# Kernel tuning notes

Hardware: AMD Instinct MI355X
Metric: run time of the kernel (lower is better)

## Reference

```python
import jax, jax.numpy as jnp
import numpy as np

IH, IW = 48, 48           # img_size
C = 256                   # inp == oup
NH, HD = 8, 32            # num_heads, head_dims; inner_dim = 256
HID = 4 * C               # MLP hidden
N = IH * IW               # window size (seq len) = 2304
SCALE = (C // NH) ** -0.5 # (inp_dims // num_heads) ** -0.5
EPS = 1e-5


def _relative_position_index():
    coords = np.stack(np.meshgrid(np.arange(IH), np.arange(IW), indexing='ij'))
    cf = coords.reshape(2, -1)
    rel = (cf[:, :, None] - cf[:, None, :]).transpose(1, 2, 0)
    rel[:, :, 0] += IH - 1
    rel[:, :, 1] += IW - 1
    rel[:, :, 0] *= 2 * IW - 1
    return jnp.asarray(rel.sum(-1).astype(np.int32))  # [N, N]


def setup_inputs() -> dict:
    key = jax.random.key(0)
    ks = jax.random.split(key, 12)
    s = 0.02
    return {
        'x': jax.random.normal(ks[0], (1, IH, IW, C), jnp.float32),
        'gamma1': jnp.ones((C,), jnp.float32),
        'beta1': jnp.zeros((C,), jnp.float32),
        'w_qkv': jax.random.normal(ks[1], (C, 3 * NH * HD), jnp.float32) * s,
        'w_proj': jax.random.normal(ks[2], (NH * HD, C), jnp.float32) * s,
        'b_proj': jnp.zeros((C,), jnp.float32),
        'bias_table': jax.random.normal(ks[3], ((2 * IH - 1) * (2 * IW - 1), NH), jnp.float32) * s,
        'gamma2': jnp.ones((C,), jnp.float32),
        'beta2': jnp.zeros((C,), jnp.float32),
        'w_fc1': jax.random.normal(ks[4], (C, HID), jnp.float32) * s,
        'b_fc1': jnp.zeros((HID,), jnp.float32),
        'w_fc2': jax.random.normal(ks[5], (HID, C), jnp.float32) * s,
        'b_fc2': jnp.zeros((C,), jnp.float32),
        'rel_idx': _relative_position_index(),
    }


def _layernorm(x, g, b):
    mu = jnp.mean(x, axis=-1, keepdims=True)
    var = jnp.mean(jnp.square(x - mu), axis=-1, keepdims=True)
    return (x - mu) * jax.lax.rsqrt(var + EPS) * g + b


def reference(x, gamma1, beta1, w_qkv, w_proj, b_proj, bias_table,
              gamma2, beta2, w_fc1, b_fc1, w_fc2, b_fc2, rel_idx):
    shortcut = x                                   # [1, IH, IW, C]
    t = x.reshape(1, N, C)
    t = _layernorm(t, gamma1, beta1)

    # qkv: [1, N, 3*NH*HD] -> q, k, v each [1, NH, N, HD]
    qkv = (t @ w_qkv).reshape(1, N, 3, NH, HD).transpose(2, 0, 3, 1, 4)
    q, k, v = qkv[0], qkv[1], qkv[2]
    q = q * SCALE

    attn = jnp.einsum('bhnd,bhmd->bhnm', q, k)     # [1, NH, N, N]
    # relative position bias: gather table rows by index -> [NH, N, N]
    bias = bias_table[rel_idx.reshape(-1)].reshape(N, N, NH).transpose(2, 0, 1)
    attn = jax.nn.softmax(attn + bias[None], axis=-1)

    o = jnp.einsum('bhnm,bhmd->bhnd', attn, v)     # [1, NH, N, HD]
    o = o.transpose(0, 2, 1, 3).reshape(1, N, NH * HD)
    o = o @ w_proj + b_proj                        # [1, N, C]

    x = shortcut + o.reshape(1, IH, IW, C)
    shortcut = x

    t = _layernorm(x.reshape(1, N, C), gamma2, beta2)
    t = jax.nn.gelu(t @ w_fc1 + b_fc1, approximate=False) @ w_fc2 + b_fc2
    return shortcut + t.reshape(1, IH, IW, C)
```

## Files before the change

### kernel.cpp

```cpp
#include <hip/hip_runtime.h>
#include <hip/hip_bf16.h>

typedef __bf16 bf16x8 __attribute__((__ext_vector_type__(8)));
typedef __bf16 bf16x4 __attribute__((__ext_vector_type__(4)));
typedef float  f32x4  __attribute__((__ext_vector_type__(4)));

#define MFMA16(a, b, c) __builtin_amdgcn_mfma_f32_16x16x32_bf16((a), (b), (c), 0, 0, 0)

static constexpr int   NSEQ  = 2304;
static constexpr float SCALE = 0.17677669529663687f;
static constexpr float LOG2E = 1.44269504088896340736f;
static constexpr int   KVS   = 6;
static constexpr float DEFER_THR = 11.5f;

#define SWZ(row, colByte) ((row) * 512 + ((colByte) ^ (((row) & 7) << 4)))

__global__ __launch_bounds__(256) void prep_kernel(
    const float* __restrict__ wqkv, const float* __restrict__ wproj,
    const float* __restrict__ wfc1, const float* __restrict__ wfc2,
    const float* __restrict__ btab,
    __hip_bfloat16* __restrict__ oqkv, __hip_bfloat16* __restrict__ oproj,
    __hip_bfloat16* __restrict__ ofc1, __hip_bfloat16* __restrict__ ofc2,
    float* __restrict__ btabT)
{
    int b = blockIdx.x;
    int tid = threadIdx.x;
    if (b >= 768) {
        int base = (b - 768) * 1024;
        for (int k = tid; k < 1024; k += 256) {
            int e = base + k;
            if (e < 72200) { int i = e >> 3, hh = e & 7; btabT[hh * 9025 + i] = btab[e] * LOG2E; }
        }
        return;
    }
    const float* src; __hip_bfloat16* dst; int K, N, t;
    if (b < 192)      { src = wqkv;  dst = oqkv;  K = 256;  N = 768;  t = b;       }
    else if (b < 256) { src = wproj; dst = oproj; K = 256;  N = 256;  t = b - 192; }
    else if (b < 512) { src = wfc1;  dst = ofc1;  K = 256;  N = 1024; t = b - 256; }
    else              { src = wfc2;  dst = ofc2;  K = 1024; N = 256;  t = b - 512; }
    int ntn = N >> 5;
    int tk = t / ntn, tn = t % ntn;
    __shared__ float tile[32][33];
    int tx = tid & 31, ty = tid >> 5;
    #pragma unroll
    for (int r = 0; r < 4; ++r)
        tile[ty + 8 * r][tx] = src[(size_t)(tk * 32 + ty + 8 * r) * N + tn * 32 + tx];
    __syncthreads();
    #pragma unroll
    for (int r = 0; r < 4; ++r)
        dst[(size_t)(tn * 32 + ty + 8 * r) * K + tk * 32 + tx] =
            __float2bfloat16(tile[tx][ty + 8 * r]);
}

__global__ __launch_bounds__(256) void qkv_ln_kernel(
    const float* __restrict__ x, const float* __restrict__ g1,
    const float* __restrict__ b1, const __hip_bfloat16* __restrict__ BT,
    __hip_bfloat16* __restrict__ Qb, __hip_bfloat16* __restrict__ Kb,
    __hip_bfloat16* __restrict__ Vt)
{
    __shared__ char smem[16 * 512];
    int tid = threadIdx.x;
    int bn = blockIdx.x * 64, bm = blockIdx.y * 16;

    {
        int row = tid >> 4, part = tid & 15;
        const float* xr = x + (size_t)(bm + row) * 256 + part * 16;
        float vals[16];
        float s = 0.f, s2 = 0.f;
        #pragma unroll
        for (int i = 0; i < 4; ++i) {
            f32x4 v4 = *reinterpret_cast<const f32x4*>(xr + 4 * i);
            #pragma unroll
            for (int e = 0; e < 4; ++e) {
                vals[4 * i + e] = v4[e];
                s += v4[e]; s2 += v4[e] * v4[e];
            }
        }
        s  += __shfl_xor(s, 1);  s  += __shfl_xor(s, 2);
        s  += __shfl_xor(s, 4);  s  += __shfl_xor(s, 8);
        s2 += __shfl_xor(s2, 1); s2 += __shfl_xor(s2, 2);
        s2 += __shfl_xor(s2, 4); s2 += __shfl_xor(s2, 8);
        float mu   = s * (1.f / 256.f);
        float var  = s2 * (1.f / 256.f) - mu * mu;
        float rstd = rsqrtf(var + 1e-5f);
        #pragma unroll
        for (int i = 0; i < 4; ++i) {
            int c = part * 16 + 4 * i;
            f32x4 gv = *reinterpret_cast<const f32x4*>(g1 + c);
            f32x4 bv = *reinterpret_cast<const f32x4*>(b1 + c);
            bf16x4 pk;
            #pragma unroll
            for (int e = 0; e < 4; ++e)
                pk[e] = (__bf16)((vals[4 * i + e] - mu) * rstd * gv[e] + bv[e]);
            *reinterpret_cast<bf16x4*>(smem + SWZ(row, c * 2)) = pk;
        }
    }
    __syncthreads();

    int w = tid >> 6, lane = tid & 63, l15 = lane & 15, g = lane >> 4;
    f32x4 acc = (f32x4){0.f, 0.f, 0.f, 0.f};
    const __hip_bfloat16* Brow = BT + (size_t)(bn + w * 16 + l15) * 256 + 8 * g;
    bf16x8 p0[2], p1[2];

#define QLOADB(dst, kb) { \
    _Pragma("unroll") for (int ks = 0; ks < 2; ++ks) \
        dst[ks] = *reinterpret_cast<const bf16x8*>(Brow + (kb) + 32 * ks); }
#define QCOMP(src, kb) { \
    _Pragma("unroll") for (int ks = 0; ks < 2; ++ks) { \
        bf16x8 af = *reinterpret_cast<const bf16x8*>(smem + SWZ(l15, 2 * ((kb) + 32 * ks + 8 * g))); \
        acc = MFMA16(af, src[ks], acc); } }

    QLOADB(p0, 0);
    QLOADB(p1, 64);
    QCOMP(p0, 0);
    QLOADB(p0, 128);
    QCOMP(p1, 64);
    QLOADB(p1, 192);
    QCOMP(p0, 128);
    QCOMP(p1, 192);
#undef QLOADB
#undef QCOMP

    if (bn >= 512) {
        __syncthreads();
        float* vtile = (float*)smem;
        #pragma unroll
        for (int j = 0; j < 4; ++j)
            vtile[(4 * g + j) * 65 + w * 16 + l15] = acc[j];
        __syncthreads();
        for (int e = tid; e < 1024; e += 256) {
            int mi = e & 15, ni = e >> 4;
            int n = bn + ni;
            int h = (n >> 5) & 7, d = n & 31;
            Vt[(size_t)(h * 32 + d) * NSEQ + bm + mi] = __float2bfloat16(vtile[mi * 65 + ni]);
        }
        return;
    }
    #pragma unroll
    for (int j = 0; j < 4; ++j) {
        int m = bm + 4 * g + j;
        int n = bn + w * 16 + l15;
        float v = acc[j];
        int which = n >> 8, h = (n >> 5) & 7, d = n & 31;
        if (which == 0) Qb[((size_t)(h * NSEQ + m) << 5) + d] = __float2bfloat16(v * (SCALE * LOG2E));
        else            Kb[((size_t)(h * NSEQ + m) << 5) + d] = __float2bfloat16(v);
    }
}

__global__ __launch_bounds__(256) void attn_kernel(
    const __hip_bfloat16* __restrict__ Q,
    const __hip_bfloat16* __restrict__ Kb,
    const __hip_bfloat16* __restrict__ Vt,
    const float* __restrict__ btabT,
    float* __restrict__ Pm, float* __restrict__ Pl,
    __hip_bfloat16* __restrict__ PO)
{
    __shared__ float bias_l[10 * 96];
    __shared__ __hip_bfloat16 P_lds[4][16][72];

    int bid = blockIdx.x;
    int h = bid / (36 * KVS);
    int r = bid - h * (36 * KVS);
    int qt = r / KVS, kvq = r - qt * KVS;
    int tid = threadIdx.x;
    int w = tid >> 6, lane = tid & 63, l15 = lane & 15, g = lane >> 4;

    int q0 = qt * 64;
    int i1min = q0 / 48, i1max = (q0 + 63) / 48;
    int dimin = i1min - (kvq * 8 + 7);
    int nrow = (i1max - i1min) + 8;

    for (int i = tid; i < nrow * 95; i += 256) {
        int rr = i / 95, cc = i - rr * 95;
        bias_l[rr * 96 + 94 - cc] = btabT[h * 9025 + (dimin + rr + 47) * 95 + cc];
    }
    __syncthreads();

    int qrow = q0 + w * 16 + l15;
    int i1 = qrow / 48, j1 = qrow - i1 * 48;
    int colBase = (i1 - dimin) * 96 + 47 - j1;
    bf16x8 qf = *reinterpret_cast<const bf16x8*>(Q + ((size_t)(h * NSEQ + qrow) << 5) + 8 * g);

    float m_st = -1e30f, l_st = 0.f;
    f32x4 o0 = (f32x4){0.f, 0.f, 0.f, 0.f};
    f32x4 o1 = (f32x4){0.f, 0.f, 0.f, 0.f};
    const f32x4 zero = (f32x4){0.f, 0.f, 0.f, 0.f};
    int kvbase = kvq * 384;

    const __hip_bfloat16* Kbase = Kb + ((size_t)(h * NSEQ + l15) << 5) + 8 * g;

    bf16x8 kf[4], kn[4];
    #pragma unroll
    for (int s = 0; s < 4; ++s)
        kn[s] = *reinterpret_cast<const bf16x8*>(Kbase + ((size_t)(kvbase + 16 * s) << 5));

    for (int t = 0; t < 6; ++t) {
        int kv0 = kvbase + t * 64;
        #pragma unroll
        for (int s = 0; s < 4; ++s) kf[s] = kn[s];
        bf16x8 vf[4];
        #pragma unroll
        for (int u = 0; u < 4; ++u) {
            int dt = u >> 1, hh = u & 1;
            vf[u] = *reinterpret_cast<const bf16x8*>(
                Vt + (size_t)((h << 5) + 16 * dt + l15) * NSEQ + kv0 + 32 * hh + 8 * g);
        }
        if (t < 5) {
            #pragma unroll
            for (int s = 0; s < 4; ++s)
                kn[s] = *reinterpret_cast<const bf16x8*>(
                    Kbase + ((size_t)(kv0 + 64 + 16 * s) << 5));
        }
        f32x4 st[4];
        #pragma unroll
        for (int s = 0; s < 4; ++s)
            st[s] = MFMA16(kf[s], qf, zero);

        float p[4][4];
        float ms[4];
        #pragma unroll
        for (int s = 0; s < 4; ++s) {
            int kvb = kv0 + 16 * s + 4 * g;
            int i2 = kvb / 48;
            int j2b = kvb - 48 * i2;
            int a0 = colBase - 96 * i2 + j2b;
            #pragma unroll
            for (int j = 0; j < 4; ++j) {
                int addr = a0 + j - ((j2b + j >= 48) ? 144 : 0);
                p[s][j] = st[s][j] + bias_l[addr];
            }
            ms[s] = fmaxf(fmaxf(p[s][0], p[s][1]), fmaxf(p[s][2], p[s][3]));
        }
        float mx = fmaxf(fmaxf(ms[0], ms[1]), fmaxf(ms[2], ms[3]));
        float mn = m_st;
        if (!__all(mx <= m_st + DEFER_THR)) {
            float mxf = fmaxf(mx, __shfl_xor(mx, 16));
            mxf = fmaxf(mxf, __shfl_xor(mxf, 32));
            mn = fmaxf(m_st, mxf);
            float sc = exp2f(m_st - mn);
            m_st = mn;
            l_st *= sc;
            float scr[4];
            #pragma unroll
            for (int j = 0; j < 4; ++j) scr[j] = __shfl(sc, 4 * g + j);
            #pragma unroll
            for (int j = 0; j < 4; ++j) { o0[j] *= scr[j]; o1[j] *= scr[j]; }
        }
        float rsum[4];
        #pragma unroll
        for (int s = 0; s < 4; ++s) {
            #pragma unroll
            for (int j = 0; j < 4; ++j) p[s][j] = exp2f(p[s][j] - mn);
            rsum[s] = (p[s][0] + p[s][1]) + (p[s][2] + p[s][3]);
        }
        l_st += (rsum[0] + rsum[1]) + (rsum[2] + rsum[3]);
        #pragma unroll
        for (int s = 0; s < 4; ++s) {
            bf16x4 pk = { (__bf16)p[s][0], (__bf16)p[s][1], (__bf16)p[s][2], (__bf16)p[s][3] };
            *reinterpret_cast<bf16x4*>(&P_lds[w][l15][16 * s + 4 * g]) = pk;
        }
        #pragma unroll
        for (int hh = 0; hh < 2; ++hh) {
            bf16x8 pf = *reinterpret_cast<const bf16x8*>(&P_lds[w][l15][32 * hh + 8 * g]);
            o0 = MFMA16(pf, vf[hh], o0);
            o1 = MFMA16(pf, vf[2 + hh], o1);
        }
    }

    float l_red = l_st + __shfl_xor(l_st, 16);
    l_red += __shfl_xor(l_red, 32);

    size_t mb = (size_t)(kvq * 8 + h) * NSEQ;
    if (g == 0) { Pm[mb + qrow] = m_st; Pl[mb + qrow] = l_red; }
    #pragma unroll
    for (int dt = 0; dt < 2; ++dt)
        #pragma unroll
        for (int j = 0; j < 4; ++j) {
            int row = q0 + w * 16 + 4 * g + j;
            PO[(mb + row) * 32 + 16 * dt + l15] =
                __float2bfloat16(dt == 0 ? o0[j] : o1[j]);
        }
}

__global__ __launch_bounds__(256) void proj_kernel(
    const __hip_bfloat16* __restrict__ PO, const float* __restrict__ Pm,
    const float* __restrict__ Pl, const __hip_bfloat16* __restrict__ BT,
    const float* __restrict__ bproj, const float* __restrict__ x,
    float* __restrict__ x2)
{
    __shared__ char smem[16 * 512];
    int tid = threadIdx.x;
    int q0 = blockIdx.y * 16, bn = blockIdx.x * 64;

    {
        int row = tid >> 4;
        int c0  = (tid & 15) * 16;
        int h = c0 >> 5, d = c0 & 31;
        float m[KVS], l[KVS], a[KVS];
        #pragma unroll
        for (int k = 0; k < KVS; ++k) {
            size_t mb = (size_t)(k * 8 + h) * NSEQ + q0 + row;
            m[k] = Pm[mb]; l[k] = Pl[mb];
        }
        float M = m[0];
        #pragma unroll
        for (int k = 1; k < KVS; ++k) M = fmaxf(M, m[k]);
        float L = 0.f;
        #pragma unroll
        for (int k = 0; k < KVS; ++k) { a[k] = exp2f(m[k] - M); L += a[k] * l[k]; }
        float inv = 1.f / L;
        float o[16];
        #pragma unroll
        for (int e = 0; e < 16; ++e) o[e] = 0.f;
        #pragma unroll
        for (int k = 0; k < KVS; ++k) {
            const __hip_bfloat16* pr = PO + ((size_t)(k * 8 + h) * NSEQ + q0 + row) * 32 + d;
            bf16x8 po0 = *reinterpret_cast<const bf16x8*>(pr);
            bf16x8 po1 = *reinterpret_cast<const bf16x8*>(pr + 8);
            #pragma unroll
            for (int e = 0; e < 8; ++e) {
                o[e]     += a[k] * (float)po0[e];
                o[8 + e] += a[k] * (float)po1[e];
            }
        }
        #pragma unroll
        for (int i = 0; i < 4; ++i) {
            bf16x4 pk;
            #pragma unroll
            for (int e = 0; e < 4; ++e) pk[e] = (__bf16)(o[4 * i + e] * inv);
            *reinterpret_cast<bf16x4*>(smem + SWZ(row, (c0 + 4 * i) * 2)) = pk;
        }
    }
    __syncthreads();

    int w = tid >> 6, lane = tid & 63, l15 = lane & 15, g = lane >> 4;
    f32x4 acc = (f32x4){0.f, 0.f, 0.f, 0.f};
    const __hip_bfloat16* Brow = BT + (size_t)(bn + w * 16 + l15) * 256 + 8 * g;
    bf16x8 p0[2], p1[2];

#define PLOADB(dst, kb) { \
    _Pragma("unroll") for (int ks = 0; ks < 2; ++ks) \
        dst[ks] = *reinterpret_cast<const bf16x8*>(Brow + (kb) + 32 * ks); }
#define PCOMP(src, kb) { \
    _Pragma("unroll") for (int ks = 0; ks < 2; ++ks) { \
        bf16x8 af = *reinterpret_cast<const bf16x8*>(smem + SWZ(l15, 2 * ((kb) + 32 * ks + 8 * g))); \
        acc = MFMA16(af, src[ks], acc); } }

    PLOADB(p0, 0);
    PLOADB(p1, 64);
    PCOMP(p0, 0);
    PLOADB(p0, 128);
    PCOMP(p1, 64);
    PLOADB(p1, 192);
    PCOMP(p0, 128);
    PCOMP(p1, 192);
#undef PLOADB
#undef PCOMP

    #pragma unroll
    for (int j = 0; j < 4; ++j) {
        int m = q0 + 4 * g + j;
        int n = bn + w * 16 + l15;
        x2[(size_t)m * 256 + n] = acc[j] + bproj[n] + x[(size_t)m * 256 + n];
    }
}

__global__ __launch_bounds__(256) void ln_fc1_kernel(
    const float* __restrict__ x2, const float* __restrict__ g2,
    const float* __restrict__ b2, const __hip_bfloat16* __restrict__ BT,
    const float* __restrict__ bfc1, __hip_bfloat16* __restrict__ hb)
{
    __shared__ char smem[32 * 512];
    int tid = threadIdx.x;
    int bn = blockIdx.x * 64, bm = blockIdx.y * 32;

    {
        int row = tid >> 3, part = tid & 7;
        const float* xr = x2 + (size_t)(bm + row) * 256 + part * 32;
        float vals[32];
        float s = 0.f, s2 = 0.f;
        #pragma unroll
        for (int i = 0; i < 8; ++i) {
            f32x4 v4 = *reinterpret_cast<const f32x4*>(xr + 4 * i);
            #pragma unroll
            for (int e = 0; e < 4; ++e) {
                vals[4 * i + e] = v4[e];
                s += v4[e]; s2 += v4[e] * v4[e];
            }
        }
        s  += __shfl_xor(s, 1);  s  += __shfl_xor(s, 2);  s  += __shfl_xor(s, 4);
        s2 += __shfl_xor(s2, 1); s2 += __shfl_xor(s2, 2); s2 += __shfl_xor(s2, 4);
        float mu   = s * (1.f / 256.f);
        float var  = s2 * (1.f / 256.f) - mu * mu;
        float rstd = rsqrtf(var + 1e-5f);
        #pragma unroll
        for (int i = 0; i < 8; ++i) {
            int c = part * 32 + 4 * i;
            f32x4 gv = *reinterpret_cast<const f32x4*>(g2 + c);
            f32x4 bv = *reinterpret_cast<const f32x4*>(b2 + c);
            bf16x4 pk;
            #pragma unroll
            for (int e = 0; e < 4; ++e)
                pk[e] = (__bf16)((vals[4 * i + e] - mu) * rstd * gv[e] + bv[e]);
            *reinterpret_cast<bf16x4*>(smem + SWZ(row, c * 2)) = pk;
        }
    }
    __syncthreads();

    int w = tid >> 6, lane = tid & 63, l15 = lane & 15, g = lane >> 4;
    int wr = w >> 1, wc = w & 1;
    f32x4 acc[2];
    acc[0] = (f32x4){0.f, 0.f, 0.f, 0.f};
    acc[1] = (f32x4){0.f, 0.f, 0.f, 0.f};
    const __hip_bfloat16* Brow = BT + (size_t)(bn + wc * 32 + l15) * 256 + 8 * g;
    bf16x8 p0[2][2], p1[2][2];

#define FLOADB(dst, kb) { \
    _Pragma("unroll") for (int ks = 0; ks < 2; ++ks) \
    _Pragma("unroll") for (int fj = 0; fj < 2; ++fj) \
        dst[ks][fj] = *reinterpret_cast<const bf16x8*>(Brow + (size_t)16 * fj * 256 + (kb) + 32 * ks); }
#define FCOMP(src, kb) { \
    _Pragma("unroll") for (int ks = 0; ks < 2; ++ks) { \
        bf16x8 af = *reinterpret_cast<const bf16x8*>(smem + SWZ(wr * 16 + l15, 2 * ((kb) + 32 * ks + 8 * g))); \
        _Pragma("unroll") for (int fj = 0; fj < 2; ++fj) \
            acc[fj] = MFMA16(af, src[ks][fj], acc[fj]); } }

    FLOADB(p0, 0);
    FLOADB(p1, 64);
    FCOMP(p0, 0);
    FLOADB(p0, 128);
    FCOMP(p1, 64);
    FLOADB(p1, 192);
    FCOMP(p0, 128);
    FCOMP(p1, 192);
#undef FLOADB
#undef FCOMP

    #pragma unroll
    for (int fj = 0; fj < 2; ++fj)
        #pragma unroll
        for (int j = 0; j < 4; ++j) {
            int m = bm + wr * 16 + 4 * g + j;
            int n = bn + wc * 32 + 16 * fj + l15;
            float r = acc[fj][j] + bfc1[n];
            float u = r * (r * r * 0.044715f + 1.f) * -2.302118131f;
            float gl = r / (1.f + exp2f(u));
            hb[(size_t)m * 1024 + n] = __float2bfloat16(gl);
        }
}

template <int KTOT, int FM, int FN, int WR, int WC>
__global__ __launch_bounds__(128) void fc2_kernel(
    const __hip_bfloat16* __restrict__ A,
    const __hip_bfloat16* __restrict__ BT,
    const float* __restrict__ bias,
    const float* __restrict__ resid,
    float* __restrict__ out0)
{
    constexpr int BM = WR * FM * 16, BN = WC * FN * 16;
    constexpr int NCH = KTOT / 64;
    constexpr int NBUF = 4;
    int bm = blockIdx.y * BM, bn = blockIdx.x * BN;
    int tid = threadIdx.x;
    int w = tid >> 6, lane = tid & 63, l15 = lane & 15, g = lane >> 4;
    int wr = w / WC, wc = w % WC;

    f32x4 acc[FM][FN];
    #pragma unroll
    for (int i = 0; i < FM; ++i)
        #pragma unroll
        for (int j = 0; j < FN; ++j) acc[i][j] = (f32x4){0.f, 0.f, 0.f, 0.f};

    const __hip_bfloat16* Arow = A  + (size_t)(bm + wr * FM * 16 + l15) * KTOT + 8 * g;
    const __hip_bfloat16* Brow = BT + (size_t)(bn + wc * FN * 16 + l15) * KTOT + 8 * g;

    bf16x8 ab[NBUF][2][FM], bb[NBUF][2][FN];

#define LOADC(ib, kb) { \
    _Pragma("unroll") for (int ks = 0; ks < 2; ++ks) { \
        _Pragma("unroll") for (int i = 0; i < FM; ++i) \
            ab[ib][ks][i] = *reinterpret_cast<const bf16x8*>(Arow + (size_t)16 * i * KTOT + (kb) + 32 * ks); \
        _Pragma("unroll") for (int j2 = 0; j2 < FN; ++j2) \
            bb[ib][ks][j2] = *reinterpret_cast<const bf16x8*>(Brow + (size_t)16 * j2 * KTOT + (kb) + 32 * ks); } }
#define COMPC(ib) { \
    _Pragma("unroll") for (int ks = 0; ks < 2; ++ks) \
        _Pragma("unroll") for (int i = 0; i < FM; ++i) \
            _Pragma("unroll") for (int j2 = 0; j2 < FN; ++j2) \
                acc[i][j2] = MFMA16(ab[ib][ks][i], bb[ib][ks][j2], acc[i][j2]); }

    #pragma unroll
    for (int ib = 0; ib < NBUF; ++ib) LOADC(ib, 64 * ib);
    #pragma unroll
    for (int t = 0; t < NCH; ++t) {
        COMPC(t % NBUF);
        if (t + NBUF < NCH) LOADC(t % NBUF, 64 * (t + NBUF));
    }
#undef LOADC
#undef COMPC

    #pragma unroll
    for (int fi = 0; fi < FM; ++fi)
    #pragma unroll
    for (int fj = 0; fj < FN; ++fj)
    #pragma unroll
    for (int j = 0; j < 4; ++j) {
        int m = bm + wr * FM * 16 + 16 * fi + 4 * g + j;
        int n = bn + wc * FN * 16 + 16 * fj + l15;
        out0[(size_t)m * 256 + n] = acc[fi][fj][j] + bias[n] + resid[(size_t)m * 256 + n];
    }
}

extern "C" void kernel_launch(void* const* d_in, const int* in_sizes, int n_in,
                              void* d_out, int out_size, void* d_ws, size_t ws_size,
                              hipStream_t stream)
{
    const float* x      = (const float*)d_in[0];
    const float* gamma1 = (const float*)d_in[1];
    const float* beta1  = (const float*)d_in[2];
    const float* w_qkv  = (const float*)d_in[3];
    const float* w_proj = (const float*)d_in[4];
    const float* b_proj = (const float*)d_in[5];
    const float* btab   = (const float*)d_in[6];
    const float* gamma2 = (const float*)d_in[7];
    const float* beta2  = (const float*)d_in[8];
    const float* w_fc1  = (const float*)d_in[9];
    const float* b_fc1  = (const float*)d_in[10];
    const float* w_fc2  = (const float*)d_in[11];
    const float* b_fc2  = (const float*)d_in[12];

    char* ws = (char*)d_ws;
    size_t off = 0;
    auto alloc = [&](size_t bytes) -> void* {
        void* p = ws + off;
        off += (bytes + 255) & ~(size_t)255;
        return p;
    };
    __hip_bfloat16* wqkvT = (__hip_bfloat16*)alloc((size_t)768 * 256 * 2);
    __hip_bfloat16* wprojT= (__hip_bfloat16*)alloc((size_t)256 * 256 * 2);
    __hip_bfloat16* wfc1T = (__hip_bfloat16*)alloc((size_t)1024 * 256 * 2);
    __hip_bfloat16* wfc2T = (__hip_bfloat16*)alloc((size_t)256 * 1024 * 2);
    float*          btabT = (float*)alloc((size_t)8 * 9025 * 4);
    __hip_bfloat16* Qb    = (__hip_bfloat16*)alloc((size_t)8 * NSEQ * 32 * 2);
    __hip_bfloat16* Kbuf  = (__hip_bfloat16*)alloc((size_t)8 * NSEQ * 32 * 2);
    __hip_bfloat16* Vt    = (__hip_bfloat16*)alloc((size_t)8 * 32 * NSEQ * 2);
    float*          x2    = (float*)alloc((size_t)NSEQ * 256 * 4);
    float*          Pm    = (float*)alloc((size_t)KVS * 8 * NSEQ * 4);
    float*          Pl    = (float*)alloc((size_t)KVS * 8 * NSEQ * 4);
    __hip_bfloat16* PO    = (__hip_bfloat16*)alloc((size_t)KVS * 8 * NSEQ * 32 * 2);
    __hip_bfloat16* hb    = (__hip_bfloat16*)alloc((size_t)NSEQ * 1024 * 2);

    prep_kernel<<<dim3(839), dim3(256), 0, stream>>>(
        w_qkv, w_proj, w_fc1, w_fc2, btab, wqkvT, wprojT, wfc1T, wfc2T, btabT);

    qkv_ln_kernel<<<dim3(12, 144), dim3(256), 0, stream>>>(
        x, gamma1, beta1, wqkvT, Qb, Kbuf, Vt);

    attn_kernel<<<dim3(8 * 36 * KVS), dim3(256), 0, stream>>>(
        Qb, Kbuf, Vt, btabT, Pm, Pl, PO);

    proj_kernel<<<dim3(4, 144), dim3(256), 0, stream>>>(
        PO, Pm, Pl, wprojT, b_proj, x, x2);

    ln_fc1_kernel<<<dim3(16, 72), dim3(256), 0, stream>>>(
        x2, gamma2, beta2, wfc1T, b_fc1, hb);

    fc2_kernel<1024, 1, 1, 2, 1><<<dim3(16, 72), dim3(128), 0, stream>>>(
        hb, wfc2T, b_fc2, x2, (float*)d_out);
}
```

Measured before the change: 196.2 us.

## Split attention KV finer, apply bias multiplicatively, split-K fc2 with atomics

Doubles the attention KV split from 6 to 12 chunks, giving more blocks with shorter loops. It also replaces the additive log-domain bias with a precomputed exp(bias) multiplier, so the running max comes from raw scores plus a margin. The fc2 GEMM becomes split-K over four slices that atomically add into an output pre-initialised by ln_fc1 with the residual plus bias. The costs are more partials for the merge step in proj, atomic contention and non-deterministic summation order, and a heuristic margin that could risk overflow for large biases.

After: 218.0 us. 1.11x slower.

```diff
diff --git a/kernel.cpp b/kernel.cpp
--- a/kernel.cpp
+++ b/kernel.cpp
@@ -10,8 +10,9 @@
 static constexpr int   NSEQ  = 2304;
 static constexpr float SCALE = 0.17677669529663687f;
 static constexpr float LOG2E = 1.44269504088896340736f;
-static constexpr int   KVS   = 6;
+static constexpr int   KVS   = 12;
 static constexpr float DEFER_THR = 11.5f;
+static constexpr float BMARGIN   = 0.25f;
 
 #define SWZ(row, colByte) ((row) * 512 + ((colByte) ^ (((row) & 7) << 4)))
 
@@ -29,7 +30,7 @@
         int base = (b - 768) * 1024;
         for (int k = tid; k < 1024; k += 256) {
             int e = base + k;
-            if (e < 72200) { int i = e >> 3, hh = e & 7; btabT[hh * 9025 + i] = btab[e] * LOG2E; }
+            if (e < 72200) { int i = e >> 3, hh = e & 7; btabT[hh * 9025 + i] = expf(btab[e]); }
         }
         return;
     }
@@ -155,7 +156,7 @@
     float* __restrict__ Pm, float* __restrict__ Pl,
     __hip_bfloat16* __restrict__ PO)
 {
-    __shared__ float bias_l[10 * 96];
+    __shared__ float bias_l[6 * 96];
     __shared__ __hip_bfloat16 P_lds[4][16][72];
 
     int bid = blockIdx.x;
@@ -167,8 +168,8 @@
 
     int q0 = qt * 64;
     int i1min = q0 / 48, i1max = (q0 + 63) / 48;
-    int dimin = i1min - (kvq * 8 + 7);
-    int nrow = (i1max - i1min) + 8;
+    int dimin = i1min - (kvq * 4 + 3);
+    int nrow = (i1max - i1min) + 4;
 
     for (int i = tid; i < nrow * 95; i += 256) {
         int rr = i / 95, cc = i - rr * 95;
@@ -185,7 +186,7 @@
     f32x4 o0 = (f32x4){0.f, 0.f, 0.f, 0.f};
     f32x4 o1 = (f32x4){0.f, 0.f, 0.f, 0.f};
     const f32x4 zero = (f32x4){0.f, 0.f, 0.f, 0.f};
-    int kvbase = kvq * 384;
+    int kvbase = kvq * 192;
 
     const __hip_bfloat16* Kbase = Kb + ((size_t)(h * NSEQ + l15) << 5) + 8 * g;
 
@@ -194,7 +195,7 @@
     for (int s = 0; s < 4; ++s)
         kn[s] = *reinterpret_cast<const bf16x8*>(Kbase + ((size_t)(kvbase + 16 * s) << 5));
 
-    for (int t = 0; t < 6; ++t) {
+    for (int t = 0; t < 3; ++t) {
         int kv0 = kvbase + t * 64;
         #pragma unroll
         for (int s = 0; s < 4; ++s) kf[s] = kn[s];
@@ -205,7 +206,7 @@
             vf[u] = *reinterpret_cast<const bf16x8*>(
                 Vt + (size_t)((h << 5) + 16 * dt + l15) * NSEQ + kv0 + 32 * hh + 8 * g);
         }
-        if (t < 5) {
+        if (t < 2) {
             #pragma unroll
             for (int s = 0; s < 4; ++s)
                 kn[s] = *reinterpret_cast<const bf16x8*>(
@@ -216,8 +217,27 @@
         for (int s = 0; s < 4; ++s)
             st[s] = MFMA16(kf[s], qf, zero);
 
-        float p[4][4];
         float ms[4];
+        #pragma unroll
+        for (int s = 0; s < 4; ++s)
+            ms[s] = fmaxf(fmaxf(st[s][0], st[s][1]), fmaxf(st[s][2], st[s][3]));
+        float mx = fmaxf(fmaxf(ms[0], ms[1]), fmaxf(ms[2], ms[3]));
+        float mn = m_st;
+        if (!__all(mx + BMARGIN <= m_st + DEFER_THR)) {
+            float mxf = fmaxf(mx, __shfl_xor(mx, 16));
+            mxf = fmaxf(mxf, __shfl_xor(mxf, 32));
+            mn = fmaxf(m_st, mxf + BMARGIN);
+            float sc = exp2f(m_st - mn);
+            m_st = mn;
+            l_st *= sc;
+            float scr[4];
+            #pragma unroll
+            for (int j = 0; j < 4; ++j) scr[j] = __shfl(sc, 4 * g + j);
+            #pragma unroll
+            for (int j = 0; j < 4; ++j) { o0[j] *= scr[j]; o1[j] *= scr[j]; }
+        }
+        float pp[4][4];
+        float rsum[4];
         #pragma unroll
         for (int s = 0; s < 4; ++s) {
             int kvb = kv0 + 16 * s + 4 * g;
@@ -227,36 +247,14 @@
             #pragma unroll
             for (int j = 0; j < 4; ++j) {
                 int addr = a0 + j - ((j2b + j >= 48) ? 144 : 0);
-                p[s][j] = st[s][j] + bias_l[addr];
+                pp[s][j] = exp2f(st[s][j] - mn) * bias_l[addr];
             }
-            ms[s] = fmaxf(fmaxf(p[s][0], p[s][1]), fmaxf(p[s][2], p[s][3]));
-        }
-        float mx = fmaxf(fmaxf(ms[0], ms[1]), fmaxf(ms[2], ms[3]));
-        float mn = m_st;
-        if (!__all(mx <= m_st + DEFER_THR)) {
-            float mxf = fmaxf(mx, __shfl_xor(mx, 16));
-            mxf = fmaxf(mxf, __shfl_xor(mxf, 32));
-            mn = fmaxf(m_st, mxf);
-            float sc = exp2f(m_st - mn);
-            m_st = mn;
-            l_st *= sc;
-            float scr[4];
-            #pragma unroll
-            for (int j = 0; j < 4; ++j) scr[j] = __shfl(sc, 4 * g + j);
-            #pragma unroll
-            for (int j = 0; j < 4; ++j) { o0[j] *= scr[j]; o1[j] *= scr[j]; }
-        }
-        float rsum[4];
+            rsum[s] = (pp[s][0] + pp[s][1]) + (pp[s][2] + pp[s][3]);
+        }
+        l_st += (rsum[0] + rsum[1]) + (rsum[2] + rsum[3]);
         #pragma unroll
         for (int s = 0; s < 4; ++s) {
-            #pragma unroll
-            for (int j = 0; j < 4; ++j) p[s][j] = exp2f(p[s][j] - mn);
-            rsum[s] = (p[s][0] + p[s][1]) + (p[s][2] + p[s][3]);
-        }
-        l_st += (rsum[0] + rsum[1]) + (rsum[2] + rsum[3]);
-        #pragma unroll
-        for (int s = 0; s < 4; ++s) {
-            bf16x4 pk = { (__bf16)p[s][0], (__bf16)p[s][1], (__bf16)p[s][2], (__bf16)p[s][3] };
+            bf16x4 pk = { (__bf16)pp[s][0], (__bf16)pp[s][1], (__bf16)pp[s][2], (__bf16)pp[s][3] };
             *reinterpret_cast<bf16x4*>(&P_lds[w][l15][16 * s + 4 * g]) = pk;
         }
         #pragma unroll
@@ -368,7 +366,8 @@
 __global__ __launch_bounds__(256) void ln_fc1_kernel(
     const float* __restrict__ x2, const float* __restrict__ g2,
     const float* __restrict__ b2, const __hip_bfloat16* __restrict__ BT,
-    const float* __restrict__ bfc1, __hip_bfloat16* __restrict__ hb)
+    const float* __restrict__ bfc1, const float* __restrict__ bfc2,
+    __hip_bfloat16* __restrict__ hb, float* __restrict__ outPre)
 {
     __shared__ char smem[32 * 512];
     int tid = threadIdx.x;
@@ -386,6 +385,17 @@
             for (int e = 0; e < 4; ++e) {
                 vals[4 * i + e] = v4[e];
                 s += v4[e]; s2 += v4[e] * v4[e];
+            }
+        }
+        if (blockIdx.x == 0) {
+            #pragma unroll
+            for (int i = 0; i < 8; ++i) {
+                int c = part * 32 + 4 * i;
+                f32x4 bv = *reinterpret_cast<const f32x4*>(bfc2 + c);
+                f32x4 ov;
+                #pragma unroll
+                for (int e = 0; e < 4; ++e) ov[e] = vals[4 * i + e] + bv[e];
+                *reinterpret_cast<f32x4*>(outPre + (size_t)(bm + row) * 256 + c) = ov;
             }
         }
         s  += __shfl_xor(s, 1);  s  += __shfl_xor(s, 2);  s  += __shfl_xor(s, 4);
@@ -449,64 +459,44 @@
         }
 }
 
-template <int KTOT, int FM, int FN, int WR, int WC>
-__global__ __launch_bounds__(128) void fc2_kernel(
+__global__ __launch_bounds__(256) void fc2_kernel(
     const __hip_bfloat16* __restrict__ A,
     const __hip_bfloat16* __restrict__ BT,
-    const float* __restrict__ bias,
-    const float* __restrict__ resid,
-    float* __restrict__ out0)
-{
-    constexpr int BM = WR * FM * 16, BN = WC * FN * 16;
-    constexpr int NCH = KTOT / 64;
-    constexpr int NBUF = 4;
-    int bm = blockIdx.y * BM, bn = blockIdx.x * BN;
+    float* __restrict__ out)
+{
+    int bm = blockIdx.y * 64, bn = blockIdx.x * 16, k0 = blockIdx.z * 256;
     int tid = threadIdx.x;
     int w = tid >> 6, lane = tid & 63, l15 = lane & 15, g = lane >> 4;
-    int wr = w / WC, wc = w % WC;
-
-    f32x4 acc[FM][FN];
-    #pragma unroll
-    for (int i = 0; i < FM; ++i)
-        #pragma unroll
-        for (int j = 0; j < FN; ++j) acc[i][j] = (f32x4){0.f, 0.f, 0.f, 0.f};
-
-    const __hip_bfloat16* Arow = A  + (size_t)(bm + wr * FM * 16 + l15) * KTOT + 8 * g;
-    const __hip_bfloat16* Brow = BT + (size_t)(bn + wc * FN * 16 + l15) * KTOT + 8 * g;
-
-    bf16x8 ab[NBUF][2][FM], bb[NBUF][2][FN];
-
-#define LOADC(ib, kb) { \
+
+    f32x4 acc = (f32x4){0.f, 0.f, 0.f, 0.f};
+    const __hip_bfloat16* Arow = A  + (size_t)(bm + w * 16 + l15) * 1024 + k0 + 8 * g;
+    const __hip_bfloat16* Brow = BT + (size_t)(bn + l15) * 1024 + k0 + 8 * g;
+
+    bf16x8 a0[2], b0[2], a1[2], b1[2];
+#define LOADC(ar, br, kb) { \
     _Pragma("unroll") for (int ks = 0; ks < 2; ++ks) { \
-        _Pragma("unroll") for (int i = 0; i < FM; ++i) \
-            ab[ib][ks][i] = *reinterpret_cast<const bf16x8*>(Arow + (size_t)16 * i * KTOT + (kb) + 32 * ks); \
-        _Pragma("unroll") for (int j2 = 0; j2 < FN; ++j2) \
-            bb[ib][ks][j2] = *reinterpret_cast<const bf16x8*>(Brow + (size_t)16 * j2 * KTOT + (kb) + 32 * ks); } }
-#define COMPC(ib) { \
+        ar[ks] = *reinterpret_cast<const bf16x8*>(Arow + (kb) + 32 * ks); \
+        br[ks] = *reinterpret_cast<const bf16x8*>(Brow + (kb) + 32 * ks); } }
+#define COMPC(ar, br) { \
     _Pragma("unroll") for (int ks = 0; ks < 2; ++ks) \
-        _Pragma("unroll") for (int i = 0; i < FM; ++i) \
-            _Pragma("unroll") for (int j2 = 0; j2 < FN; ++j2) \
-                acc[i][j2] = MFMA16(ab[ib][ks][i], bb[ib][ks][j2], acc[i][j2]); }
-
-    #pragma unroll
-    for (int ib = 0; ib < NBUF; ++ib) LOADC(ib, 64 * ib);
-    #pragma unroll
-    for (int t = 0; t < NCH; ++t) {
-        COMPC(t % NBUF);
-        if (t + NBUF < NCH) LOADC(t % NBUF, 64 * (t + NBUF));
-    }
+        acc = MFMA16(ar[ks], br[ks], acc); }
+
+    LOADC(a0, b0, 0);
+    LOADC(a1, b1, 64);
+    COMPC(a0, b0);
+    LOADC(a0, b0, 128);
+    COMPC(a1, b1);
+    LOADC(a1, b1, 192);
+    COMPC(a0, b0);
+    COMPC(a1, b1);
 #undef LOADC
 #undef COMPC
 
     #pragma unroll
-    for (int fi = 0; fi < FM; ++fi)
-    #pragma unroll
-    for (int fj = 0; fj < FN; ++fj)
-    #pragma unroll
     for (int j = 0; j < 4; ++j) {
-        int m = bm + wr * FM * 16 + 16 * fi + 4 * g + j;
-        int n = bn + wc * FN * 16 + 16 * fj + l15;
-        out0[(size_t)m * 256 + n] = acc[fi][fj][j] + bias[n] + resid[(size_t)m * 256 + n];
+        int m = bm + w * 16 + 4 * g + j;
+        int n = bn + l15;
+        atomicAdd(out + (size_t)m * 256 + n, acc[j]);
     }
 }
 
@@ -562,8 +552,8 @@
         PO, Pm, Pl, wprojT, b_proj, x, x2);
 
     ln_fc1_kernel<<<dim3(16, 72), dim3(256), 0, stream>>>(
-        x2, gamma2, beta2, wfc1T, b_fc1, hb);
-
-    fc2_kernel<1024, 1, 1, 2, 1><<<dim3(16, 72), dim3(128), 0, stream>>>(
-        hb, wfc2T, b_fc2, x2, (float*)d_out);
-}
+        x2, gamma2, beta2, wfc1T, b_fc1, b_fc2, hb, (float*)d_out);
+
+    fc2_kernel<<<dim3(16, 36, 4), dim3(256), 0, stream>>>(
+        hb, wfc2T, (float*)d_out);
+}
```
